# Kernel tuning notes

Hardware: AMD Instinct MI355X
Metric: run time of the kernel (lower is better)

## Reference

```python
import jax, jax.numpy as jnp
import numpy as np

MAX_STEPS = 20  # matches init kwarg max_steps


def gru_cell(x, h, W_ih, W_hh, b_ih, b_hh):
    # PyTorch GRUCell: gates ordered (reset, update, new)
    H = h.shape[1]
    gx = x @ W_ih.T + b_ih          # [B, 3H]
    gh = h @ W_hh.T + b_hh          # [B, 3H]
    r = jax.nn.sigmoid(gx[:, :H] + gh[:, :H])
    z = jax.nn.sigmoid(gx[:, H:2 * H] + gh[:, H:2 * H])
    n = jnp.tanh(gx[:, 2 * H:] + r * gh[:, 2 * H:])
    return (1.0 - z) * n + z * h


def setup_inputs() -> dict:
    key = jax.random.key(0)
    ks = jax.random.split(key, 10)
    B, E, H = 2048, 512, 1024
    bound = 1.0 / np.sqrt(H)  # torch default init scale
    uni = lambda k, shape: jax.random.uniform(k, shape, jnp.float32, -bound, bound)
    return {
        "x": jax.random.normal(ks[0], (B, E), jnp.float32),
        "W_ih": uni(ks[1], (3 * H, E)),
        "W_hh": uni(ks[2], (3 * H, H)),
        "b_ih": uni(ks[3], (3 * H,)),
        "b_hh": uni(ks[4], (3 * H,)),
        "w_out": uni(ks[5], (H,)),
        "b_out": uni(ks[6], (1,)),
        "w_lam": uni(ks[7], (H,)),
        "b_lam": uni(ks[8], (1,)),
        "u": jax.random.uniform(ks[9], (MAX_STEPS, B), jnp.float32),  # bernoulli draws
    }


def reference(x, W_ih, W_hh, b_ih, b_hh, w_out, b_out, w_lam, b_lam, u):
    B = x.shape[0]
    dt = x.dtype
    H = W_hh.shape[1]
    h0 = gru_cell(x, jnp.zeros((B, H), dt), W_ih, W_hh, b_ih, b_hh)
    steps = jnp.arange(1, MAX_STEPS + 1)

    def step(carry, inp):
        h, un_halted, halted, p_m, y_m = carry
        n_idx, u_n = inp
        lam_sig = jax.nn.sigmoid(h @ w_lam + b_lam[0])           # [B]
        lam = jnp.where(n_idx == MAX_STEPS, jnp.ones_like(lam_sig), lam_sig)
        y_n = h @ w_out + b_out[0]                                # [B]
        p_n = un_halted * lam
        un_halted = un_halted * (1.0 - lam)
        halt = (u_n < lam).astype(dt) * (1.0 - halted)            # bernoulli(lam)
        p_m = p_m * (1.0 - halt) + p_n * halt
        y_m = y_m * (1.0 - halt) + y_n * halt
        halted = halted + halt
        h = gru_cell(x, h, W_ih, W_hh, b_ih, b_hh)
        return (h, un_halted, halted, p_m, y_m), (p_n, y_n)

    init = (h0,
            jnp.ones((B,), dt),
            jnp.zeros((B,), dt),
            jnp.zeros((B,), dt),
            jnp.zeros((B,), dt))
    (_, _, _, p_m, y_m), (p, y) = jax.lax.scan(step, init, (steps, u))
    return p, y, p_m, y_m
```

## Files before the change

### kernel.cpp

```cpp
#include <hip/hip_runtime.h>
#include <math.h>


#define B_N 2048
#define E_N 512
#define H_N 1024
#define G3  3072
#define NSTEPS 20
#define BK 32
#define NT_H (H_N / BK)
#define NT_E (E_N / BK)
#define NCB  (H_N / 32)

typedef __attribute__((ext_vector_type(8))) _Float16 f16x8;
typedef __attribute__((ext_vector_type(4))) _Float16 f16x4v;
typedef __attribute__((ext_vector_type(4))) float    f32x4;

#define GLDS(src, dst) \
  __builtin_amdgcn_global_load_lds( \
      (const __attribute__((address_space(1))) void*)(src), \
      (__attribute__((address_space(3))) void*)(dst), 16, 0, 0)

__device__ __forceinline__ float sigmoidf_(float x) { return 1.0f / (1.0f + expf(-x)); }

__global__ __launch_bounds__(256, 2)
void gemm_step_mfma(const _Float16* __restrict__ h_hi_in,
                    const _Float16* __restrict__ h_lo_in,
                    const _Float16* __restrict__ Whi,
                    const _Float16* __restrict__ Wlo,
                    const float* __restrict__ b_hh,
                    const float* __restrict__ gx,
                    const float* __restrict__ w_lam,
                    const float* __restrict__ w_out,
                    _Float16* __restrict__ h_hi_out,
                    _Float16* __restrict__ h_lo_out,
                    float* __restrict__ part_lam,
                    float* __restrict__ part_out)
{
  __shared__ _Float16 lds[2][14336];
  __shared__ float pl_red[128][2], po_red[128][2];

  const int tid  = threadIdx.x;
  const int lane = tid & 63;
  const int wv   = tid >> 6;
  const int wr   = wv >> 1;
  const int wc   = wv & 1;
  const int row0 = blockIdx.y * 128;
  const int col0 = blockIdx.x * 32;
  const int cb   = blockIdx.x;

  const _Float16* srcp[7];
  int ldsoff[7];
  #pragma unroll
  for (int j = 0; j < 7; ++j) {
    const int c     = wv * 7 + j;
    const int seg   = (lane & 3) * 8;
    const int row16 = lane >> 2;
    const _Float16* s;
    if (c < 8) {
      s = h_hi_in + (size_t)(row0 + c * 16 + row16) * H_N + seg;
    } else if (c < 16) {
      s = h_lo_in + (size_t)(row0 + (c - 8) * 16 + row16) * H_N + seg;
    } else if (c < 22) {
      const int br = (c - 16) * 16 + row16;
      s = Whi + (size_t)((br >> 5) * H_N + col0 + (br & 31)) * H_N + seg;
    } else {
      const int br = (c - 22) * 16 + row16;
      s = Wlo + (size_t)((br >> 5) * H_N + col0 + (br & 31)) * H_N + seg;
    }
    srcp[j]   = s;
    ldsoff[j] = c * 512;
  }

  f32x4 acc[3][4];
  #pragma unroll
  for (int g = 0; g < 3; ++g)
    #pragma unroll
    for (int mi = 0; mi < 4; ++mi)
      acc[g][mi] = (f32x4){0.f, 0.f, 0.f, 0.f};

  const int lrow = lane & 15;
  const int lk   = (lane >> 4) * 8;
  const int q    = lane >> 4;

  #pragma unroll
  for (int j = 0; j < 7; ++j) { GLDS(srcp[j], &lds[0][ldsoff[j]]); srcp[j] += BK; }
  __syncthreads();

  for (int t = 0; t < NT_H; ++t) {
    const int p = t & 1;
    if (t + 1 < NT_H) {
      #pragma unroll
      for (int j = 0; j < 7; ++j) { GLDS(srcp[j], &lds[p ^ 1][ldsoff[j]]); srcp[j] += BK; }
    }
    f16x8 ah[4], al[4];
    #pragma unroll
    for (int mi = 0; mi < 4; ++mi) {
      const int r = wr * 64 + mi * 16 + lrow;
      ah[mi] = *(const f16x8*)&lds[p][r * 32 + lk];
      al[mi] = *(const f16x8*)&lds[p][4096 + r * 32 + lk];
    }
    f16x8 bh[3], bl[3];
    #pragma unroll
    for (int g = 0; g < 3; ++g) {
      const int r = g * 32 + wc * 16 + lrow;
      bh[g] = *(const f16x8*)&lds[p][8192 + r * 32 + lk];
      bl[g] = *(const f16x8*)&lds[p][11264 + r * 32 + lk];
    }
    #pragma unroll
    for (int g = 0; g < 3; ++g)
      #pragma unroll
      for (int mi = 0; mi < 4; ++mi) {
        f32x4 c = acc[g][mi];
        c = __builtin_amdgcn_mfma_f32_16x16x32_f16(ah[mi], bh[g], c, 0, 0, 0);
        c = __builtin_amdgcn_mfma_f32_16x16x32_f16(ah[mi], bl[g], c, 0, 0, 0);
        c = __builtin_amdgcn_mfma_f32_16x16x32_f16(al[mi], bh[g], c, 0, 0, 0);
        acc[g][mi] = c;
      }
    __syncthreads();
  }

  const int n   = col0 + wc * 16 + lrow;
  const float bhr = b_hh[n];
  const float bhz = b_hh[H_N + n];
  const float bhn = b_hh[2 * H_N + n];
  const float wl  = w_lam[n];
  const float wo  = w_out[n];
  #pragma unroll
  for (int mi = 0; mi < 4; ++mi) {
    #pragma unroll
    for (int r = 0; r < 4; ++r) {
      const int m = row0 + wr * 64 + mi * 16 + q * 4 + r;
      const float gr = acc[0][mi][r] + bhr;
      const float gz = acc[1][mi][r] + bhz;
      const float gn = acc[2][mi][r] + bhn;
      const size_t gxb = (size_t)m * G3;
      const float rr = sigmoidf_(gx[gxb + n] + gr);
      const float zz = sigmoidf_(gx[gxb + H_N + n] + gz);
      const float nn = tanhf(gx[gxb + 2 * H_N + n] + rr * gn);
      const size_t hidx = (size_t)m * H_N + n;
      const float hold = (float)h_hi_in[hidx] + (float)h_lo_in[hidx];
      const float hf = (1.f - zz) * nn + zz * hold;
      const _Float16 hh = (_Float16)hf;
      h_hi_out[hidx] = hh;
      h_lo_out[hidx] = (_Float16)(hf - (float)hh);
      float pl = hf * wl;
      float po = hf * wo;
      #pragma unroll
      for (int mk = 1; mk < 16; mk <<= 1) {
        pl += __shfl_xor(pl, mk);
        po += __shfl_xor(po, mk);
      }
      if (lrow == 0) {
        pl_red[wr * 64 + mi * 16 + q * 4 + r][wc] = pl;
        po_red[wr * 64 + mi * 16 + q * 4 + r][wc] = po;
      }
    }
  }
  __syncthreads();
  if (tid < 128) {
    const int m = row0 + tid;
    part_lam[(size_t)cb * B_N + m] = pl_red[tid][0] + pl_red[tid][1];
    part_out[(size_t)cb * B_N + m] = po_red[tid][0] + po_red[tid][1];
  }
}

__global__ __launch_bounds__(256, 3)
void gemm_gx_mfma(const _Float16* __restrict__ xhi,
                  const _Float16* __restrict__ xlo,
                  const _Float16* __restrict__ Wihhi,
                  const _Float16* __restrict__ Wihlo,
                  const float* __restrict__ b_ih,
                  float* __restrict__ gx)
{
  __shared__ _Float16 lds[2][12288];

  const int tid  = threadIdx.x;
  const int lane = tid & 63;
  const int wv   = tid >> 6;
  const int wr   = wv >> 1;
  const int wc   = wv & 1;
  const int row0 = blockIdx.y * 128;
  const int col0 = blockIdx.x * 64;

  const _Float16* srcp[6];
  int ldsoff[6];
  #pragma unroll
  for (int j = 0; j < 6; ++j) {
    const int c     = wv * 6 + j;
    const int seg   = (lane & 3) * 8;
    const int row16 = lane >> 2;
    const _Float16* s;
    if (c < 8)       s = xhi   + (size_t)(row0 + c * 16 + row16) * E_N + seg;
    else if (c < 16) s = xlo   + (size_t)(row0 + (c - 8) * 16 + row16) * E_N + seg;
    else if (c < 20) s = Wihhi + (size_t)(col0 + (c - 16) * 16 + row16) * E_N + seg;
    else             s = Wihlo + (size_t)(col0 + (c - 20) * 16 + row16) * E_N + seg;
    srcp[j]   = s;
    ldsoff[j] = c * 512;
  }

  f32x4 acc[4][2];
  #pragma unroll
  for (int mi = 0; mi < 4; ++mi)
    #pragma unroll
    for (int ni = 0; ni < 2; ++ni) acc[mi][ni] = (f32x4){0.f, 0.f, 0.f, 0.f};

  const int lrow = lane & 15;
  const int lk   = (lane >> 4) * 8;
  const int q    = lane >> 4;

  #pragma unroll
  for (int j = 0; j < 6; ++j) { GLDS(srcp[j], &lds[0][ldsoff[j]]); srcp[j] += BK; }
  __syncthreads();

  for (int t = 0; t < NT_E; ++t) {
    const int p = t & 1;
    if (t + 1 < NT_E) {
      #pragma unroll
      for (int j = 0; j < 6; ++j) { GLDS(srcp[j], &lds[p ^ 1][ldsoff[j]]); srcp[j] += BK; }
    }
    f16x8 ah[4], al[4];
    #pragma unroll
    for (int mi = 0; mi < 4; ++mi) {
      const int r = wr * 64 + mi * 16 + lrow;
      ah[mi] = *(const f16x8*)&lds[p][r * 32 + lk];
      al[mi] = *(const f16x8*)&lds[p][4096 + r * 32 + lk];
    }
    f16x8 bh[2], bl[2];
    #pragma unroll
    for (int ni = 0; ni < 2; ++ni) {
      const int r = wc * 32 + ni * 16 + lrow;
      bh[ni] = *(const f16x8*)&lds[p][8192 + r * 32 + lk];
      bl[ni] = *(const f16x8*)&lds[p][10240 + r * 32 + lk];
    }
    #pragma unroll
    for (int mi = 0; mi < 4; ++mi)
      #pragma unroll
      for (int ni = 0; ni < 2; ++ni) {
        f32x4 c = acc[mi][ni];
        c = __builtin_amdgcn_mfma_f32_16x16x32_f16(ah[mi], bh[ni], c, 0, 0, 0);
        c = __builtin_amdgcn_mfma_f32_16x16x32_f16(ah[mi], bl[ni], c, 0, 0, 0);
        c = __builtin_amdgcn_mfma_f32_16x16x32_f16(al[mi], bh[ni], c, 0, 0, 0);
        acc[mi][ni] = c;
      }
    __syncthreads();
  }

  #pragma unroll
  for (int mi = 0; mi < 4; ++mi) {
    #pragma unroll
    for (int ni = 0; ni < 2; ++ni) {
      const int n = col0 + wc * 32 + ni * 16 + lrow;
      const float bi = b_ih[n];
      #pragma unroll
      for (int r = 0; r < 4; ++r) {
        const int m = row0 + wr * 64 + mi * 16 + q * 4 + r;
        gx[(size_t)m * G3 + n] = acc[mi][ni][r] + bi;
      }
    }
  }
}

__global__ __launch_bounds__(256)
void split_f32_kernel(const float* __restrict__ src,
                      _Float16* __restrict__ hi, _Float16* __restrict__ lo)
{
  const size_t base = ((size_t)blockIdx.x * 256 + threadIdx.x) * 4;
  const float4 w = *(const float4*)&src[base];
  float s[4] = {w.x, w.y, w.z, w.w};
  f16x4v h4, l4;
  #pragma unroll
  for (int e = 0; e < 4; ++e) {
    const _Float16 h = (_Float16)s[e];
    h4[e] = h;
    l4[e] = (_Float16)(s[e] - (float)h);
  }
  *(f16x4v*)&hi[base] = h4;
  *(f16x4v*)&lo[base] = l4;
}

__global__ __launch_bounds__(256)
void init_h0_kernel(const float* __restrict__ gx, const float* __restrict__ b_hh,
                    _Float16* __restrict__ h_hi, _Float16* __restrict__ h_lo,
                    float* __restrict__ states)
{
    const int idx = blockIdx.x * 256 + threadIdx.x;
    const int r = idx >> 10;
    const int c = idx & (H_N - 1);
    const float rr = sigmoidf_(gx[(size_t)r * G3 + c] + b_hh[c]);
    const float zz = sigmoidf_(gx[(size_t)r * G3 + H_N + c] + b_hh[H_N + c]);
    const float nn = tanhf(gx[(size_t)r * G3 + 2 * H_N + c] + rr * b_hh[2 * H_N + c]);
    const float hf = (1.0f - zz) * nn;
    const _Float16 hh = (_Float16)hf;
    h_hi[idx] = hh;
    h_lo[idx] = (_Float16)(hf - (float)hh);
    if (idx < B_N) {
        states[idx]           = 1.0f;
        states[B_N + idx]     = 0.0f;
        states[2 * B_N + idx] = 0.0f;
        states[3 * B_N + idx] = 0.0f;
    }
}

__global__ __launch_bounds__(256)
void halt_kernel(const int n,
                 const _Float16* __restrict__ h_hi, const _Float16* __restrict__ h_lo,
                 const float* __restrict__ w_out, const float* __restrict__ b_out,
                 const float* __restrict__ w_lam, const float* __restrict__ b_lam,
                 const float* __restrict__ u,
                 float* __restrict__ states,
                 float* __restrict__ out_p, float* __restrict__ out_y,
                 float* __restrict__ out_pm, float* __restrict__ out_ym)
{
    const int row = blockIdx.x;
    const int tid = threadIdx.x;
    const size_t base = (size_t)row * H_N + (tid << 2);
    const f16x4v hh4 = *(const f16x4v*)&h_hi[base];
    const f16x4v hl4 = *(const f16x4v*)&h_lo[base];
    const float4 wl = *(const float4*)&w_lam[tid << 2];
    const float4 wo = *(const float4*)&w_out[tid << 2];
    float hv[4];
    #pragma unroll
    for (int e = 0; e < 4; ++e) hv[e] = (float)hh4[e] + (float)hl4[e];
    float s_lam = hv[0] * wl.x + hv[1] * wl.y + hv[2] * wl.z + hv[3] * wl.w;
    float s_out = hv[0] * wo.x + hv[1] * wo.y + hv[2] * wo.z + hv[3] * wo.w;
    #pragma unroll
    for (int off = 32; off > 0; off >>= 1) {
        s_lam += __shfl_down(s_lam, off);
        s_out += __shfl_down(s_out, off);
    }
    __shared__ float redl[4], redo[4];
    const int wid = tid >> 6;
    if ((tid & 63) == 0) { redl[wid] = s_lam; redo[wid] = s_out; }
    __syncthreads();
    if (tid == 0) {
        const float dlam = redl[0] + redl[1] + redl[2] + redl[3];
        const float dout = redo[0] + redo[1] + redo[2] + redo[3];
        const float lam = (n == NSTEPS) ? 1.0f : sigmoidf_(dlam + b_lam[0]);
        const float y_n = dout + b_out[0];
        float un = states[row];
        float ha = states[B_N + row];
        float pm = states[2 * B_N + row];
        float ym = states[3 * B_N + row];
        const float p_n = un * lam;
        un = un * (1.0f - lam);
        const float halt = (u[(size_t)(n - 1) * B_N + row] < lam ? 1.0f : 0.0f) * (1.0f - ha);
        pm = pm * (1.0f - halt) + p_n * halt;
        ym = ym * (1.0f - halt) + y_n * halt;
        ha += halt;
        states[row] = un;
        states[B_N + row] = ha;
        states[2 * B_N + row] = pm;
        states[3 * B_N + row] = ym;
        out_p[(size_t)(n - 1) * B_N + row] = p_n;
        out_y[(size_t)(n - 1) * B_N + row] = y_n;
        if (n == NSTEPS) { out_pm[row] = pm; out_ym[row] = ym; }
    }
}

__global__ __launch_bounds__(256)
void finish_halt_kernel(const int n,
                        const float* __restrict__ part_lam,
                        const float* __restrict__ part_out,
                        const float* __restrict__ b_out, const float* __restrict__ b_lam,
                        const float* __restrict__ u,
                        float* __restrict__ states,
                        float* __restrict__ out_p, float* __restrict__ out_y,
                        float* __restrict__ out_pm, float* __restrict__ out_ym)
{
    const int row = blockIdx.x * 256 + threadIdx.x;
    float dlam = 0.f, dout = 0.f;
    #pragma unroll
    for (int cb = 0; cb < NCB; ++cb) {
        dlam += part_lam[(size_t)cb * B_N + row];
        dout += part_out[(size_t)cb * B_N + row];
    }
    const float lam = (n == NSTEPS) ? 1.0f : sigmoidf_(dlam + b_lam[0]);
    const float y_n = dout + b_out[0];
    float un = states[row];
    float ha = states[B_N + row];
    float pm = states[2 * B_N + row];
    float ym = states[3 * B_N + row];
    const float p_n = un * lam;
    un = un * (1.0f - lam);
    const float halt = (u[(size_t)(n - 1) * B_N + row] < lam ? 1.0f : 0.0f) * (1.0f - ha);
    pm = pm * (1.0f - halt) + p_n * halt;
    ym = ym * (1.0f - halt) + y_n * halt;
    ha += halt;
    states[row] = un;
    states[B_N + row] = ha;
    states[2 * B_N + row] = pm;
    states[3 * B_N + row] = ym;
    out_p[(size_t)(n - 1) * B_N + row] = p_n;
    out_y[(size_t)(n - 1) * B_N + row] = y_n;
    if (n == NSTEPS) { out_pm[row] = pm; out_ym[row] = ym; }
}

extern "C" void kernel_launch(void* const* d_in, const int* in_sizes, int n_in,
                              void* d_out, int out_size, void* d_ws, size_t ws_size,
                              hipStream_t stream) {
    const float* x     = (const float*)d_in[0];
    const float* W_ih  = (const float*)d_in[1];
    const float* W_hh  = (const float*)d_in[2];
    const float* b_ih  = (const float*)d_in[3];
    const float* b_hh  = (const float*)d_in[4];
    const float* w_out = (const float*)d_in[5];
    const float* b_out = (const float*)d_in[6];
    const float* w_lam = (const float*)d_in[7];
    const float* b_lam = (const float*)d_in[8];
    const float* u     = (const float*)d_in[9];

    float* out_p  = (float*)d_out;
    float* out_y  = out_p + (size_t)NSTEPS * B_N;
    float* out_pm = out_y + (size_t)NSTEPS * B_N;
    float* out_ym = out_pm + B_N;

    float* ws = (float*)d_ws;
    float*     gx   = ws;
    _Float16*  Whi  = (_Float16*)(gx + (size_t)B_N * G3);
    _Float16*  Wlo  = Whi + (size_t)G3 * H_N;
    _Float16*  hAhi = Wlo + (size_t)G3 * H_N;
    _Float16*  hAlo = hAhi + (size_t)B_N * H_N;
    _Float16*  hBhi = hAlo + (size_t)B_N * H_N;
    _Float16*  hBlo = hBhi + (size_t)B_N * H_N;
    float*     part_lam = (float*)(hBlo + (size_t)B_N * H_N);
    float*     part_out = part_lam + (size_t)NCB * B_N;
    float*     states   = part_out + (size_t)NCB * B_N;

    const dim3 blk(256);
    split_f32_kernel<<<dim3((size_t)G3 * H_N / 1024), blk, 0, stream>>>(W_hh, Whi, Wlo);
    split_f32_kernel<<<dim3((size_t)G3 * E_N / 1024), blk, 0, stream>>>(W_ih, hAhi, hAlo);
    split_f32_kernel<<<dim3((size_t)B_N * E_N / 1024), blk, 0, stream>>>(x, hBhi, hBlo);
    gemm_gx_mfma<<<dim3(G3 / 64, B_N / 128), blk, 0, stream>>>(hBhi, hBlo, hAhi, hAlo, b_ih, gx);
    init_h0_kernel<<<dim3(B_N * H_N / 256), blk, 0, stream>>>(gx, b_hh, hAhi, hAlo, states);

    _Float16 *hchi = hAhi, *hclo = hAlo, *hnhi = hBhi, *hnlo = hBlo;
    for (int n = 1; n <= NSTEPS; ++n) {
        if (n == 1) {
            halt_kernel<<<dim3(B_N), blk, 0, stream>>>(n, hchi, hclo, w_out, b_out,
                                                       w_lam, b_lam, u, states,
                                                       out_p, out_y, out_pm, out_ym);
        } else {
            finish_halt_kernel<<<dim3(B_N / 256), blk, 0, stream>>>(n, part_lam, part_out,
                                                                    b_out, b_lam, u, states,
                                                                    out_p, out_y, out_pm, out_ym);
        }
        if (n < NSTEPS) {
            gemm_step_mfma<<<dim3(H_N / 32, B_N / 128), blk, 0, stream>>>(
                hchi, hclo, Whi, Wlo, b_hh, gx, w_lam, w_out, hnhi, hnlo, part_lam, part_out);
            _Float16* t;
            t = hchi; hchi = hnhi; hnhi = t;
            t = hclo; hclo = hnlo; hnlo = t;
        }
    }
}
```

Before: 1.286 ms.

## Widen step GEMM tile to 64 columns with triple-buffered LDS pipeline

The recurrent GEMM block now covers 64 output columns with 512 threads (8 waves), which halves the number of column blocks and the redundant reloads of the h tile. The LDS pipeline moves from double to triple buffering with explicit vmcnt waits and a single barrier per k-step. An XOR swizzle is applied to the LDS layout to cut bank conflicts. The previous hidden state is now read from LDS during the matching k-tile instead of from global memory in the epilogue. The larger LDS footprint (about 120KB) and the bigger block may lower occupancy, and the manual wait counts must match the number of loads issued per stage.

```diff
diff --git a/kernel.cpp b/kernel.cpp
--- a/kernel.cpp
+++ b/kernel.cpp
@@ -10,7 +10,7 @@
 #define BK 32
 #define NT_H (H_N / BK)
 #define NT_E (E_N / BK)
-#define NCB  (H_N / 32)
+#define NCB  (H_N / 64)
 
 typedef __attribute__((ext_vector_type(8))) _Float16 f16x8;
 typedef __attribute__((ext_vector_type(4))) _Float16 f16x4v;
@@ -23,7 +23,7 @@
 
 __device__ __forceinline__ float sigmoidf_(float x) { return 1.0f / (1.0f + expf(-x)); }
 
-__global__ __launch_bounds__(256, 2)
+__global__ __launch_bounds__(512, 2)
 void gemm_step_mfma(const _Float16* __restrict__ h_hi_in,
                     const _Float16* __restrict__ h_lo_in,
                     const _Float16* __restrict__ Whi,
@@ -37,36 +37,37 @@
                     float* __restrict__ part_lam,
                     float* __restrict__ part_out)
 {
-  __shared__ _Float16 lds[2][14336];
-  __shared__ float pl_red[128][2], po_red[128][2];
+  __shared__ _Float16 lds[3][20480];
+  __shared__ float pl_red[128][4], po_red[128][4];
 
   const int tid  = threadIdx.x;
   const int lane = tid & 63;
   const int wv   = tid >> 6;
-  const int wr   = wv >> 1;
-  const int wc   = wv & 1;
+  const int wr   = wv >> 2;
+  const int wc   = wv & 3;
   const int row0 = blockIdx.y * 128;
-  const int col0 = blockIdx.x * 32;
+  const int col0 = blockIdx.x * 64;
   const int cb   = blockIdx.x;
 
-  const _Float16* srcp[7];
-  int ldsoff[7];
-  #pragma unroll
-  for (int j = 0; j < 7; ++j) {
-    const int c     = wv * 7 + j;
-    const int seg   = (lane & 3) * 8;
+  const _Float16* srcp[5];
+  int ldsoff[5];
+  #pragma unroll
+  for (int j = 0; j < 5; ++j) {
+    const int c     = wv * 5 + j;
     const int row16 = lane >> 2;
+    const int seg16 = lane & 3;
+    const int seg   = (seg16 ^ (row16 & 3)) * 8;
     const _Float16* s;
     if (c < 8) {
       s = h_hi_in + (size_t)(row0 + c * 16 + row16) * H_N + seg;
     } else if (c < 16) {
       s = h_lo_in + (size_t)(row0 + (c - 8) * 16 + row16) * H_N + seg;
-    } else if (c < 22) {
+    } else if (c < 28) {
       const int br = (c - 16) * 16 + row16;
-      s = Whi + (size_t)((br >> 5) * H_N + col0 + (br & 31)) * H_N + seg;
+      s = Whi + (size_t)((br >> 6) * H_N + col0 + (br & 63)) * H_N + seg;
     } else {
-      const int br = (c - 22) * 16 + row16;
-      s = Wlo + (size_t)((br >> 5) * H_N + col0 + (br & 31)) * H_N + seg;
+      const int br = (c - 28) * 16 + row16;
+      s = Wlo + (size_t)((br >> 6) * H_N + col0 + (br & 63)) * H_N + seg;
     }
     srcp[j]   = s;
     ldsoff[j] = c * 512;
@@ -80,32 +81,45 @@
       acc[g][mi] = (f32x4){0.f, 0.f, 0.f, 0.f};
 
   const int lrow = lane & 15;
-  const int lk   = (lane >> 4) * 8;
   const int q    = lane >> 4;
-
-  #pragma unroll
-  for (int j = 0; j < 7; ++j) { GLDS(srcp[j], &lds[0][ldsoff[j]]); srcp[j] += BK; }
-  __syncthreads();
-
-  for (int t = 0; t < NT_H; ++t) {
-    const int p = t & 1;
-    if (t + 1 < NT_H) {
-      #pragma unroll
-      for (int j = 0; j < 7; ++j) { GLDS(srcp[j], &lds[p ^ 1][ldsoff[j]]); srcp[j] += BK; }
-    }
+  const int lkp  = (q ^ (lrow & 3)) * 8;
+  const int capT = 2 * cb + (wc >> 1);
+  float hold[4][4];
+
+  auto issue = [&](int slot) {
+    #pragma unroll
+    for (int j = 0; j < 5; ++j) { GLDS(srcp[j], &lds[slot][ldsoff[j]]); srcp[j] += BK; }
+  };
+
+  auto body = [&](int t, bool do_issue) {
+    __builtin_amdgcn_s_barrier();
+    __builtin_amdgcn_sched_barrier(0);
+    if (do_issue) issue((t + 2) % 3);
+    const int sl = t % 3;
     f16x8 ah[4], al[4];
     #pragma unroll
     for (int mi = 0; mi < 4; ++mi) {
       const int r = wr * 64 + mi * 16 + lrow;
-      ah[mi] = *(const f16x8*)&lds[p][r * 32 + lk];
-      al[mi] = *(const f16x8*)&lds[p][4096 + r * 32 + lk];
+      ah[mi] = *(const f16x8*)&lds[sl][r * 32 + lkp];
+      al[mi] = *(const f16x8*)&lds[sl][4096 + r * 32 + lkp];
     }
     f16x8 bh[3], bl[3];
     #pragma unroll
     for (int g = 0; g < 3; ++g) {
-      const int r = g * 32 + wc * 16 + lrow;
-      bh[g] = *(const f16x8*)&lds[p][8192 + r * 32 + lk];
-      bl[g] = *(const f16x8*)&lds[p][11264 + r * 32 + lk];
+      const int br = g * 64 + wc * 16 + lrow;
+      bh[g] = *(const f16x8*)&lds[sl][8192 + br * 32 + lkp];
+      bl[g] = *(const f16x8*)&lds[sl][14336 + br * 32 + lkp];
+    }
+    if (t == capT) {
+      #pragma unroll
+      for (int mi = 0; mi < 4; ++mi)
+        #pragma unroll
+        for (int r = 0; r < 4; ++r) {
+          const int arow = wr * 64 + mi * 16 + q * 4 + r;
+          const int sslt = (((wc & 1) * 2 + (lrow >> 3)) ^ r) * 8 + (lrow & 7);
+          hold[mi][r] = (float)lds[sl][arow * 32 + sslt]
+                      + (float)lds[sl][4096 + arow * 32 + sslt];
+        }
     }
     #pragma unroll
     for (int g = 0; g < 3; ++g)
@@ -117,8 +131,16 @@
         c = __builtin_amdgcn_mfma_f32_16x16x32_f16(al[mi], bh[g], c, 0, 0, 0);
         acc[g][mi] = c;
       }
-    __syncthreads();
-  }
+  };
+
+  issue(0);
+  issue(1);
+  for (int t = 0; t < NT_H - 1; ++t) {
+    asm volatile("s_waitcnt vmcnt(5)" ::: "memory");
+    body(t, t < NT_H - 2);
+  }
+  asm volatile("s_waitcnt vmcnt(0)" ::: "memory");
+  body(NT_H - 1, false);
 
   const int n   = col0 + wc * 16 + lrow;
   const float bhr = b_hh[n];
@@ -138,10 +160,9 @@
       const float rr = sigmoidf_(gx[gxb + n] + gr);
       const float zz = sigmoidf_(gx[gxb + H_N + n] + gz);
       const float nn = tanhf(gx[gxb + 2 * H_N + n] + rr * gn);
+      const float hf = (1.f - zz) * nn + zz * hold[mi][r];
+      const _Float16 hh = (_Float16)hf;
       const size_t hidx = (size_t)m * H_N + n;
-      const float hold = (float)h_hi_in[hidx] + (float)h_lo_in[hidx];
-      const float hf = (1.f - zz) * nn + zz * hold;
-      const _Float16 hh = (_Float16)hf;
       h_hi_out[hidx] = hh;
       h_lo_out[hidx] = (_Float16)(hf - (float)hh);
       float pl = hf * wl;
@@ -160,8 +181,10 @@
   __syncthreads();
   if (tid < 128) {
     const int m = row0 + tid;
-    part_lam[(size_t)cb * B_N + m] = pl_red[tid][0] + pl_red[tid][1];
-    part_out[(size_t)cb * B_N + m] = po_red[tid][0] + po_red[tid][1];
+    part_lam[(size_t)cb * B_N + m] = (pl_red[tid][0] + pl_red[tid][1])
+                                   + (pl_red[tid][2] + pl_red[tid][3]);
+    part_out[(size_t)cb * B_N + m] = (po_red[tid][0] + po_red[tid][1])
+                                   + (po_red[tid][2] + po_red[tid][3]);
   }
 }
 
@@ -446,7 +469,7 @@
                                                                     out_p, out_y, out_pm, out_ym);
         }
         if (n < NSTEPS) {
-            gemm_step_mfma<<<dim3(H_N / 32, B_N / 128), blk, 0, stream>>>(
+            gemm_step_mfma<<<dim3(H_N / 64, B_N / 128), dim3(512), 0, stream>>>(
                 hchi, hclo, Whi, Wlo, b_hh, gx, w_lam, w_out, hnhi, hnlo, part_lam, part_out);
             _Float16* t;
             t = hchi; hchi = hnhi; hnhi = t;
```

Result: no change. 1.280 ms (-0.5%).

## Widen recurrent GEMM tile to 64 columns with triple-buffered LDS pipeline

Applied to the files above, without the earlier changes.

The per-step recurrent GEMM now computes 64 hidden columns per block instead of 32, so each loaded h tile is reused across twice as many columns. The double-buffered loop with full syncthreads is replaced by a three-slot LDS ring using explicit vmcnt waits and a single barrier, keeping two tiles in flight. The LDS layout is rearranged so MFMA fragments are read contiguously, and the previous h value for the epilogue is read from LDS during the matching K tile instead of from global memory. In exchange, LDS and register use grow and occupancy drops to one block per SIMD set, and the grid is halved to 256 blocks.

```diff
diff --git a/kernel.cpp b/kernel.cpp
--- a/kernel.cpp
+++ b/kernel.cpp
@@ -10,7 +10,7 @@
 #define BK 32
 #define NT_H (H_N / BK)
 #define NT_E (E_N / BK)
-#define NCB  (H_N / 32)
+#define NCB  (H_N / 64)
 
 typedef __attribute__((ext_vector_type(8))) _Float16 f16x8;
 typedef __attribute__((ext_vector_type(4))) _Float16 f16x4v;
@@ -23,7 +23,7 @@
 
 __device__ __forceinline__ float sigmoidf_(float x) { return 1.0f / (1.0f + expf(-x)); }
 
-__global__ __launch_bounds__(256, 2)
+__global__ __launch_bounds__(256, 1)
 void gemm_step_mfma(const _Float16* __restrict__ h_hi_in,
                     const _Float16* __restrict__ h_lo_in,
                     const _Float16* __restrict__ Whi,
@@ -37,7 +37,7 @@
                     float* __restrict__ part_lam,
                     float* __restrict__ part_out)
 {
-  __shared__ _Float16 lds[2][14336];
+  __shared__ _Float16 lds[3][20480];
   __shared__ float pl_red[128][2], po_red[128][2];
 
   const int tid  = threadIdx.x;
@@ -46,106 +46,147 @@
   const int wr   = wv >> 1;
   const int wc   = wv & 1;
   const int row0 = blockIdx.y * 128;
-  const int col0 = blockIdx.x * 32;
+  const int col0 = blockIdx.x * 64;
   const int cb   = blockIdx.x;
 
-  const _Float16* srcp[7];
-  int ldsoff[7];
-  #pragma unroll
-  for (int j = 0; j < 7; ++j) {
-    const int c     = wv * 7 + j;
-    const int seg   = (lane & 3) * 8;
-    const int row16 = lane >> 2;
+  const int lrow = lane & 15;
+  const int q    = lane >> 4;
+
+  const _Float16* srcp[10];
+  int ldsoff[10];
+  #pragma unroll
+  for (int j = 0; j < 10; ++j) {
+    const int c   = wv * 10 + j;
+    const int lrx = lane & 15;
+    const int qx  = lane >> 4;
     const _Float16* s;
     if (c < 8) {
-      s = h_hi_in + (size_t)(row0 + c * 16 + row16) * H_N + seg;
+      const int row = row0 + (c >> 2) * 64 + (c & 3) * 16 + lrx;
+      s = h_hi_in + (size_t)row * H_N + qx * 8;
     } else if (c < 16) {
-      s = h_lo_in + (size_t)(row0 + (c - 8) * 16 + row16) * H_N + seg;
-    } else if (c < 22) {
-      const int br = (c - 16) * 16 + row16;
-      s = Whi + (size_t)((br >> 5) * H_N + col0 + (br & 31)) * H_N + seg;
+      const int cc = c - 8;
+      const int row = row0 + (cc >> 2) * 64 + (cc & 3) * 16 + lrx;
+      s = h_lo_in + (size_t)row * H_N + qx * 8;
+    } else if (c < 28) {
+      const int cc = c - 16;
+      const int rowg = (cc >> 2) * H_N + col0 + (cc & 3) * 16 + lrx;
+      s = Whi + (size_t)rowg * H_N + qx * 8;
     } else {
-      const int br = (c - 22) * 16 + row16;
-      s = Wlo + (size_t)((br >> 5) * H_N + col0 + (br & 31)) * H_N + seg;
+      const int cc = c - 28;
+      const int rowg = (cc >> 2) * H_N + col0 + (cc & 3) * 16 + lrx;
+      s = Wlo + (size_t)rowg * H_N + qx * 8;
     }
     srcp[j]   = s;
     ldsoff[j] = c * 512;
   }
 
-  f32x4 acc[3][4];
+  f32x4 acc[3][4][2];
   #pragma unroll
   for (int g = 0; g < 3; ++g)
     #pragma unroll
     for (int mi = 0; mi < 4; ++mi)
-      acc[g][mi] = (f32x4){0.f, 0.f, 0.f, 0.f};
-
-  const int lrow = lane & 15;
-  const int lk   = (lane >> 4) * 8;
-  const int q    = lane >> 4;
-
-  #pragma unroll
-  for (int j = 0; j < 7; ++j) { GLDS(srcp[j], &lds[0][ldsoff[j]]); srcp[j] += BK; }
-  __syncthreads();
+      #pragma unroll
+      for (int ni = 0; ni < 2; ++ni)
+        acc[g][mi][ni] = (f32x4){0.f, 0.f, 0.f, 0.f};
+
+  const int capT = 2 * cb + wc;
+  float hold[4][2][4];
+
+  auto issue = [&](int slot) {
+    #pragma unroll
+    for (int j = 0; j < 10; ++j) { GLDS(srcp[j], &lds[slot][ldsoff[j]]); srcp[j] += BK; }
+  };
+
+  issue(0);
+  issue(1);
 
   for (int t = 0; t < NT_H; ++t) {
-    const int p = t & 1;
-    if (t + 1 < NT_H) {
-      #pragma unroll
-      for (int j = 0; j < 7; ++j) { GLDS(srcp[j], &lds[p ^ 1][ldsoff[j]]); srcp[j] += BK; }
-    }
+    if (t < NT_H - 1) asm volatile("s_waitcnt vmcnt(10)" ::: "memory");
+    else              asm volatile("s_waitcnt vmcnt(0)"  ::: "memory");
+    __builtin_amdgcn_s_barrier();
+    if (t + 2 < NT_H) issue((t + 2) % 3);
+    __builtin_amdgcn_sched_barrier(0);
+
+    const _Float16* Lp = &lds[t % 3][0];
+
     f16x8 ah[4], al[4];
     #pragma unroll
     for (int mi = 0; mi < 4; ++mi) {
-      const int r = wr * 64 + mi * 16 + lrow;
-      ah[mi] = *(const f16x8*)&lds[p][r * 32 + lk];
-      al[mi] = *(const f16x8*)&lds[p][4096 + r * 32 + lk];
-    }
-    f16x8 bh[3], bl[3];
-    #pragma unroll
-    for (int g = 0; g < 3; ++g) {
-      const int r = g * 32 + wc * 16 + lrow;
-      bh[g] = *(const f16x8*)&lds[p][8192 + r * 32 + lk];
-      bl[g] = *(const f16x8*)&lds[p][11264 + r * 32 + lk];
-    }
+      const int u = ((wr * 4 + mi) * 64 + lane) * 8;
+      ah[mi] = *(const f16x8*)&Lp[u];
+      al[mi] = *(const f16x8*)&Lp[4096 + u];
+    }
+    f16x8 bh[3][2], bl[3][2];
     #pragma unroll
     for (int g = 0; g < 3; ++g)
       #pragma unroll
-      for (int mi = 0; mi < 4; ++mi) {
-        f32x4 c = acc[g][mi];
-        c = __builtin_amdgcn_mfma_f32_16x16x32_f16(ah[mi], bh[g], c, 0, 0, 0);
-        c = __builtin_amdgcn_mfma_f32_16x16x32_f16(ah[mi], bl[g], c, 0, 0, 0);
-        c = __builtin_amdgcn_mfma_f32_16x16x32_f16(al[mi], bh[g], c, 0, 0, 0);
-        acc[g][mi] = c;
-      }
-    __syncthreads();
-  }
-
-  const int n   = col0 + wc * 16 + lrow;
-  const float bhr = b_hh[n];
-  const float bhz = b_hh[H_N + n];
-  const float bhn = b_hh[2 * H_N + n];
-  const float wl  = w_lam[n];
-  const float wo  = w_out[n];
+      for (int ni = 0; ni < 2; ++ni) {
+        const int u = ((g * 4 + wc * 2 + ni) * 64 + lane) * 8;
+        bh[g][ni] = *(const f16x8*)&Lp[8192 + u];
+        bl[g][ni] = *(const f16x8*)&Lp[14336 + u];
+      }
+
+    if (t == capT) {
+      #pragma unroll
+      for (int mi = 0; mi < 4; ++mi)
+        #pragma unroll
+        for (int ni = 0; ni < 2; ++ni)
+          #pragma unroll
+          for (int r = 0; r < 4; ++r) {
+            const int unit = (wr * 4 + mi) * 64 + (ni * 2 + (lrow >> 3)) * 16 + q * 4 + r;
+            const int off  = unit * 8 + (lrow & 7);
+            hold[mi][ni][r] = (float)Lp[off] + (float)Lp[4096 + off];
+          }
+    }
+
+    #pragma unroll
+    for (int g = 0; g < 3; ++g)
+      #pragma unroll
+      for (int mi = 0; mi < 4; ++mi)
+        #pragma unroll
+        for (int ni = 0; ni < 2; ++ni) {
+          f32x4 c = acc[g][mi][ni];
+          c = __builtin_amdgcn_mfma_f32_16x16x32_f16(ah[mi], bh[g][ni], c, 0, 0, 0);
+          c = __builtin_amdgcn_mfma_f32_16x16x32_f16(ah[mi], bl[g][ni], c, 0, 0, 0);
+          c = __builtin_amdgcn_mfma_f32_16x16x32_f16(al[mi], bh[g][ni], c, 0, 0, 0);
+          acc[g][mi][ni] = c;
+        }
+  }
+
   #pragma unroll
   for (int mi = 0; mi < 4; ++mi) {
+    float plr[4] = {0.f, 0.f, 0.f, 0.f};
+    float por[4] = {0.f, 0.f, 0.f, 0.f};
+    #pragma unroll
+    for (int ni = 0; ni < 2; ++ni) {
+      const int n = col0 + wc * 32 + ni * 16 + lrow;
+      const float bhr = b_hh[n];
+      const float bhz = b_hh[H_N + n];
+      const float bhn = b_hh[2 * H_N + n];
+      const float wl  = w_lam[n];
+      const float wo  = w_out[n];
+      #pragma unroll
+      for (int r = 0; r < 4; ++r) {
+        const int m = row0 + wr * 64 + mi * 16 + q * 4 + r;
+        const float gr = acc[0][mi][ni][r] + bhr;
+        const float gz = acc[1][mi][ni][r] + bhz;
+        const float gn = acc[2][mi][ni][r] + bhn;
+        const size_t gxb = (size_t)m * G3;
+        const float rr = sigmoidf_(gx[gxb + n] + gr);
+        const float zz = sigmoidf_(gx[gxb + H_N + n] + gz);
+        const float nn = tanhf(gx[gxb + 2 * H_N + n] + rr * gn);
+        const float hf = (1.f - zz) * nn + zz * hold[mi][ni][r];
+        const _Float16 hh = (_Float16)hf;
+        const size_t hidx = (size_t)m * H_N + n;
+        h_hi_out[hidx] = hh;
+        h_lo_out[hidx] = (_Float16)(hf - (float)hh);
+        plr[r] += hf * wl;
+        por[r] += hf * wo;
+      }
+    }
     #pragma unroll
     for (int r = 0; r < 4; ++r) {
-      const int m = row0 + wr * 64 + mi * 16 + q * 4 + r;
-      const float gr = acc[0][mi][r] + bhr;
-      const float gz = acc[1][mi][r] + bhz;
-      const float gn = acc[2][mi][r] + bhn;
-      const size_t gxb = (size_t)m * G3;
-      const float rr = sigmoidf_(gx[gxb + n] + gr);
-      const float zz = sigmoidf_(gx[gxb + H_N + n] + gz);
-      const float nn = tanhf(gx[gxb + 2 * H_N + n] + rr * gn);
-      const size_t hidx = (size_t)m * H_N + n;
-      const float hold = (float)h_hi_in[hidx] + (float)h_lo_in[hidx];
-      const float hf = (1.f - zz) * nn + zz * hold;
-      const _Float16 hh = (_Float16)hf;
-      h_hi_out[hidx] = hh;
-      h_lo_out[hidx] = (_Float16)(hf - (float)hh);
-      float pl = hf * wl;
-      float po = hf * wo;
+      float pl = plr[r], po = por[r];
       #pragma unroll
       for (int mk = 1; mk < 16; mk <<= 1) {
         pl += __shfl_xor(pl, mk);
@@ -446,7 +487,7 @@
                                                                     out_p, out_y, out_pm, out_ym);
         }
         if (n < NSTEPS) {
-            gemm_step_mfma<<<dim3(H_N / 32, B_N / 128), blk, 0, stream>>>(
+            gemm_step_mfma<<<dim3(H_N / 64, B_N / 128), blk, 0, stream>>>(
                 hchi, hclo, Whi, Wlo, b_hh, gx, w_lam, w_out, hnhi, hnlo, part_lam, part_out);
             _Float16* t;
             t = hchi; hchi = hnhi; hnhi = t;
```

Result: slower. 1.630 ms (+26.7%).
